# Kernel tuning notes

Measured on AMD Instinct MI355X. Metric: run time of the kernel, lower is better.

Reference implementation:

```python
import jax, jax.numpy as jnp
import numpy as np

N_AUTHOR, N_SUBJECT, N_PAPER = 200000, 50000, 100000
E = 1000000
D = 64
NEG_SLOPE = 0.01


def setup_inputs() -> dict:
    key = jax.random.key(0)
    ks = jax.random.split(key, 16)
    return {
        "feat_author": jax.random.normal(ks[0], (N_AUTHOR, D), jnp.float32),
        "feat_subject": jax.random.normal(ks[1], (N_SUBJECT, D), jnp.float32),
        "feat_paper": jax.random.normal(ks[2], (N_PAPER, D), jnp.float32),
        "edge_src_ap": jax.random.randint(ks[3], (E,), 0, N_AUTHOR, jnp.int32),
        "edge_dst_ap": jax.random.randint(ks[4], (E,), 0, N_PAPER, jnp.int32),
        "edge_src_sp": jax.random.randint(ks[5], (E,), 0, N_SUBJECT, jnp.int32),
        "edge_dst_sp": jax.random.randint(ks[6], (E,), 0, N_PAPER, jnp.int32),
        "attn_l_ap": jax.random.normal(ks[7], (D,), jnp.float32) * 0.1,
        "attn_r_ap": jax.random.normal(ks[8], (D,), jnp.float32) * 0.1,
        "attn_l_sp": jax.random.normal(ks[9], (D,), jnp.float32) * 0.1,
        "attn_r_sp": jax.random.normal(ks[10], (D,), jnp.float32) * 0.1,
        "fc_w": jax.random.normal(ks[11], (D, D), jnp.float32) * 0.1,
        "fc_b": jax.random.normal(ks[12], (D,), jnp.float32) * 0.1,
        "sem_attn": jax.random.normal(ks[13], (D,), jnp.float32) * 0.1,
    }


def heco_gat(feat_src, feat_dst, attn_l, attn_r, src, dst, n_dst):
    # per-node attention logits
    el = feat_src @ attn_l          # [Ns]
    er = feat_dst @ attn_r          # [Nd]
    e = el[src] + er[dst]           # [E]
    e = jnp.where(e > 0, e, NEG_SLOPE * e)  # leaky_relu
    # edge softmax grouped by destination node (numerically stable)
    emax = jax.ops.segment_max(e, dst, num_segments=n_dst)
    ee = jnp.exp(e - emax[dst])
    denom = jax.ops.segment_sum(ee, dst, num_segments=n_dst)
    a = ee / denom[dst]             # [E]
    # weighted scatter-sum aggregation
    out = jax.ops.segment_sum(a[:, None] * feat_src[src], dst, num_segments=n_dst)
    return jax.nn.elu(out)


def semantic_attention(h, fc_w, fc_b, sem_attn):
    # h: [N, M, d]
    w = jnp.tanh(h @ fc_w.T + fc_b).mean(axis=0) @ sem_attn  # [M]
    beta = jax.nn.softmax(w)                                  # [M]
    return jnp.einsum("m,nmd->nd", beta, h)


def reference(feat_author, feat_subject, feat_paper,
              edge_src_ap, edge_dst_ap, edge_src_sp, edge_dst_sp,
              attn_l_ap, attn_r_ap, attn_l_sp, attn_r_sp,
              fc_w, fc_b, sem_attn):
    n_dst = feat_paper.shape[0]
    h_ap = heco_gat(feat_author, feat_paper, attn_l_ap, attn_r_ap,
                    edge_src_ap, edge_dst_ap, n_dst)
    h_sp = heco_gat(feat_subject, feat_paper, attn_l_sp, attn_r_sp,
                    edge_src_sp, edge_dst_sp, n_dst)
    h = jnp.stack([h_ap, h_sp], axis=1)  # [N_dst, 2, D]
    return semantic_attention(h, fc_w, fc_b, sem_attn)
```

## Files before the change

kernel.cpp:

```cpp
#include <hip/hip_runtime.h>
#include <math.h>

#define N_AUTHOR 200000
#define N_SUBJECT 50000
#define N_PAPER 100000
#define NEDGE 1000000
#define D 64
#define NEG_SLOPE 0.01f

#define NSLOT (2 * N_PAPER)
#define CAP 40
#define DROWS (N_AUTHOR + N_SUBJECT + N_PAPER)

__device__ __forceinline__ float bcast(float v, int lane) {
    return __uint_as_float((unsigned)__builtin_amdgcn_readlane(__float_as_int(v), lane));
}
__device__ __forceinline__ int bcast_i(int v, int lane) {
    return __builtin_amdgcn_readlane(v, lane);
}
__device__ __forceinline__ float fast_tanh(float x) {
    x = fminf(15.0f, fmaxf(-15.0f, x));
    float ex = __expf(2.0f * x);
    return (ex - 1.0f) / (ex + 1.0f);
}


__global__ void dots_scatter_kernel(const float* __restrict__ fa,
                                    const float* __restrict__ fs,
                                    const float* __restrict__ fp,
                                    const float* __restrict__ al_ap,
                                    const float* __restrict__ ar_ap,
                                    const float* __restrict__ al_sp,
                                    const float* __restrict__ ar_sp,
                                    float* __restrict__ el_ap,
                                    float* __restrict__ el_sp,
                                    float* __restrict__ er_ap,
                                    float* __restrict__ er_sp,
                                    const int* __restrict__ src_ap,
                                    const int* __restrict__ dst_ap,
                                    const int* __restrict__ src_sp,
                                    const int* __restrict__ dst_sp,
                                    int* __restrict__ count,
                                    int* __restrict__ bucket,
                                    int nb_dots) {
    if ((int)blockIdx.x < nb_dots) {
        int row  = blockIdx.x * 4 + (threadIdx.x >> 6);
        int lane = threadIdx.x & 63;
        if (row < N_AUTHOR) {
            float v = fa[(size_t)row * D + lane] * al_ap[lane];
#pragma unroll
            for (int o = 32; o > 0; o >>= 1) v += __shfl_xor(v, o, 64);
            if (lane == 0) el_ap[row] = v;
        } else if (row < N_AUTHOR + N_SUBJECT) {
            int r = row - N_AUTHOR;
            float v = fs[(size_t)r * D + lane] * al_sp[lane];
#pragma unroll
            for (int o = 32; o > 0; o >>= 1) v += __shfl_xor(v, o, 64);
            if (lane == 0) el_sp[r] = v;
        } else if (row < DROWS) {
            int r = row - (N_AUTHOR + N_SUBJECT);
            float f  = fp[(size_t)r * D + lane];
            float v0 = f * ar_ap[lane];
            float v1 = f * ar_sp[lane];
#pragma unroll
            for (int o = 32; o > 0; o >>= 1) {
                v0 += __shfl_xor(v0, o, 64);
                v1 += __shfl_xor(v1, o, 64);
            }
            if (lane == 0) { er_ap[r] = v0; er_sp[r] = v1; }
        }
    } else {
        const int nthreads = 2 * NEDGE / 4;
        int tid = (blockIdx.x - nb_dots) * blockDim.x + threadIdx.x;
        if (tid >= nthreads) return;
#pragma unroll
        for (int k = 0; k < 4; ++k) {
            int i = tid + k * nthreads;
            int s, dslot;
            if (i < NEDGE) {
                s = src_ap[i];
                dslot = dst_ap[i];
            } else {
                int j = i - NEDGE;
                s = src_sp[j];
                dslot = N_PAPER + dst_sp[j];
            }
            int pos = atomicAdd(&count[dslot], 1);
            if (pos < CAP) bucket[dslot * CAP + pos] = s;
        }
    }
}

__global__ void __launch_bounds__(256, 4)
node_gat_fused_kernel(const int* __restrict__ count,
                      const int* __restrict__ bucket,
                      const float* __restrict__ el_ap,
                      const float* __restrict__ el_sp,
                      const float* __restrict__ er_ap,
                      const float* __restrict__ er_sp,
                      const float* __restrict__ feat_author,
                      const float* __restrict__ feat_subject,
                      float* __restrict__ h_ap,
                      float* __restrict__ h_sp,
                      const float* __restrict__ fc_w,
                      const float* __restrict__ fc_b,
                      const float* __restrict__ sem_attn,
                      float* __restrict__ wsum) {
    __shared__ float red[8];
    int wid  = threadIdx.x >> 6;
    int lane = threadIdx.x & 63;

    float fw[D];
    {
        const float4* fw4 = (const float4*)(fc_w + (size_t)lane * D);
#pragma unroll
        for (int k = 0; k < 16; ++k) {
            float4 v = fw4[k];
            fw[4 * k + 0] = v.x; fw[4 * k + 1] = v.y;
            fw[4 * k + 2] = v.z; fw[4 * k + 3] = v.w;
        }
    }
    float fb = fc_b[lane];
    float sa = sem_attn[lane];
    float taccL0 = 0.0f, taccL1 = 0.0f;

    for (int slot = blockIdx.x * 4 + wid; slot < NSLOT; slot += gridDim.x * 4) {
        int mp = slot >= N_PAPER;
        const float* feat = mp ? feat_subject : feat_author;
        const float* el   = mp ? el_sp : el_ap;
        float er_s = mp ? er_sp[slot - N_PAPER] : er_ap[slot];
        int len = count[slot];
        len = len < CAP ? len : CAP;

        int   sreg = 0;
        float ev   = -1e30f;
        if (lane < len) {
            sreg = bucket[slot * CAP + lane];
            float e = el[sreg] + er_s;
            ev = e > 0.0f ? e : NEG_SLOPE * e;
        }
        float m = ev;
#pragma unroll
        for (int o = 32; o > 0; o >>= 1) m = fmaxf(m, __shfl_xor(m, o, 64));
        float w = (lane < len) ? __expf(ev - m) : 0.0f;
        float sden = w;
#pragma unroll
        for (int o = 32; o > 0; o >>= 1) sden += __shfl_xor(sden, o, 64);

        float a0 = 0.0f, a1 = 0.0f, a2 = 0.0f, a3 = 0.0f;
        int j = 0;
        for (; j + 4 <= len; j += 4) {
            float w0 = bcast(w, j),     w1 = bcast(w, j + 1);
            float w2 = bcast(w, j + 2), w3 = bcast(w, j + 3);
            int   s0 = bcast_i(sreg, j),     s1 = bcast_i(sreg, j + 1);
            int   s2 = bcast_i(sreg, j + 2), s3 = bcast_i(sreg, j + 3);
            a0 = fmaf(w0, feat[(size_t)s0 * D + lane], a0);
            a1 = fmaf(w1, feat[(size_t)s1 * D + lane], a1);
            a2 = fmaf(w2, feat[(size_t)s2 * D + lane], a2);
            a3 = fmaf(w3, feat[(size_t)s3 * D + lane], a3);
        }
        for (; j < len; ++j) {
            float w0 = bcast(w, j);
            int   s0 = bcast_i(sreg, j);
            a0 = fmaf(w0, feat[(size_t)s0 * D + lane], a0);
        }
        float hpre = len ? (((a0 + a1) + (a2 + a3)) / sden) : 0.0f;
        float hv = hpre > 0.0f ? hpre : (__expf(hpre) - 1.0f);

        float* h = mp ? (h_sp + (size_t)(slot - N_PAPER) * D)
                      : (h_ap + (size_t)slot * D);
        h[lane] = hv;

        float m0 = 0.0f, m1 = 0.0f, m2 = 0.0f, m3 = 0.0f;
#pragma unroll
        for (int dd = 0; dd < D; dd += 4) {
            m0 = fmaf(bcast(hv, dd),     fw[dd],     m0);
            m1 = fmaf(bcast(hv, dd + 1), fw[dd + 1], m1);
            m2 = fmaf(bcast(hv, dd + 2), fw[dd + 2], m2);
            m3 = fmaf(bcast(hv, dd + 3), fw[dd + 3], m3);
        }
        float y = fb + ((m0 + m1) + (m2 + m3));
        float t = fast_tanh(y) * sa;
        if (mp) taccL1 += t; else taccL0 += t;
    }

#pragma unroll
    for (int o = 32; o > 0; o >>= 1) {
        taccL0 += __shfl_xor(taccL0, o, 64);
        taccL1 += __shfl_xor(taccL1, o, 64);
    }
    if (lane == 0) { red[wid] = taccL0; red[4 + wid] = taccL1; }
    __syncthreads();
    if (threadIdx.x == 0) atomicAdd(&wsum[0], red[0] + red[1] + red[2] + red[3]);
    if (threadIdx.x == 1) atomicAdd(&wsum[1], red[4] + red[5] + red[6] + red[7]);
}

__global__ void final_combine_kernel(float4* __restrict__ out,
                                     const float4* __restrict__ h_sp,
                                     const float* __restrict__ wsum,
                                     int n_vec4) {
    int i = blockIdx.x * blockDim.x + threadIdx.x;
    if (i >= n_vec4) return;
    float w0 = wsum[0] * (1.0f / N_PAPER);
    float w1 = wsum[1] * (1.0f / N_PAPER);
    float mx = fmaxf(w0, w1);
    float e0 = __expf(w0 - mx), e1 = __expf(w1 - mx);
    float inv = 1.0f / (e0 + e1);
    float b0 = e0 * inv, b1 = e1 * inv;
    float4 a = out[i], b = h_sp[i];
    out[i] = make_float4(b0 * a.x + b1 * b.x, b0 * a.y + b1 * b.y,
                         b0 * a.z + b1 * b.z, b0 * a.w + b1 * b.w);
}


extern "C" void kernel_launch(void* const* d_in, const int* in_sizes, int n_in,
                              void* d_out, int out_size, void* d_ws, size_t ws_size,
                              hipStream_t stream) {
    const float* feat_author = (const float*)d_in[0];
    const float* feat_subject= (const float*)d_in[1];
    const float* feat_paper  = (const float*)d_in[2];
    const int*   src_ap      = (const int*)d_in[3];
    const int*   dst_ap      = (const int*)d_in[4];
    const int*   src_sp      = (const int*)d_in[5];
    const int*   dst_sp      = (const int*)d_in[6];
    const float* attn_l_ap   = (const float*)d_in[7];
    const float* attn_r_ap   = (const float*)d_in[8];
    const float* attn_l_sp   = (const float*)d_in[9];
    const float* attn_r_sp   = (const float*)d_in[10];
    const float* fc_w        = (const float*)d_in[11];
    const float* fc_b        = (const float*)d_in[12];
    const float* sem_attn    = (const float*)d_in[13];

    float* out = (float*)d_out;

    char* ws = (char*)d_ws;
    size_t off = 0;
    auto alloc = [&](size_t bytes) {
        size_t r = off;
        off = (off + bytes + 255) & ~(size_t)255;
        return r;
    };
    int*   count  = (int*)(ws + alloc((size_t)NSLOT * 4));
    float* wsum   = (float*)(ws + alloc(2 * 4));
    size_t zero_bytes = off;
    float* el_ap  = (float*)(ws + alloc((size_t)N_AUTHOR * 4));
    float* er_ap  = (float*)(ws + alloc((size_t)N_PAPER * 4));
    float* el_sp  = (float*)(ws + alloc((size_t)N_SUBJECT * 4));
    float* er_sp  = (float*)(ws + alloc((size_t)N_PAPER * 4));
    int*   bucket = (int*)(ws + alloc((size_t)NSLOT * CAP * 4));
    float* h_sp   = (float*)(ws + alloc((size_t)N_PAPER * D * 4));
    (void)ws_size; (void)in_sizes; (void)n_in;

    hipMemsetAsync(d_ws, 0, zero_bytes, stream);

    const int B = 256;

    int nb_dots    = (DROWS + 3) / 4;
    int nb_scatter = (2 * NEDGE / 4 + B - 1) / B;
    dots_scatter_kernel<<<nb_dots + nb_scatter, B, 0, stream>>>(
        feat_author, feat_subject, feat_paper,
        attn_l_ap, attn_r_ap, attn_l_sp, attn_r_sp,
        el_ap, el_sp, er_ap, er_sp,
        src_ap, dst_ap, src_sp, dst_sp,
        count, bucket, nb_dots);

    node_gat_fused_kernel<<<2048, B, 0, stream>>>(count, bucket,
                                                  el_ap, el_sp, er_ap, er_sp,
                                                  feat_author, feat_subject,
                                                  out, h_sp,
                                                  fc_w, fc_b, sem_attn, wsum);

    int n_vec4 = N_PAPER * D / 4;
    final_combine_kernel<<<(n_vec4 + B - 1) / B, B, 0, stream>>>(
        (float4*)out, (const float4*)h_sp, wsum, n_vec4);
}
```

Measured before the change: 538.4 us.

## Split metapath pipeline to overlap subject-edge scatter with author-paper GAT

Restructures the launch sequence into three kernels. The first scatters author-paper edges and computes the node dot products. The second scatters subject-paper edges while other blocks run GAT aggregation for the author metapath. The third runs GAT for the subject metapath. This lets atomic scatter work overlap with gather/aggregation work instead of serialising all scatter before all GAT. It also switches bucket writes to nontemporal stores. The cost is an extra kernel launch and a duplicated fc_w register load per kernel.

```diff
diff --git a/kernel.cpp b/kernel.cpp
--- a/kernel.cpp
+++ b/kernel.cpp
@@ -11,6 +11,7 @@
 #define NSLOT (2 * N_PAPER)
 #define CAP 40
 #define DROWS (N_AUTHOR + N_SUBJECT + N_PAPER)
+#define NB_SCAT 977
 
 __device__ __forceinline__ float bcast(float v, int lane) {
     return __uint_as_float((unsigned)__builtin_amdgcn_readlane(__float_as_int(v), lane));
@@ -24,92 +25,143 @@
     return (ex - 1.0f) / (ex + 1.0f);
 }
 
-
-__global__ void dots_scatter_kernel(const float* __restrict__ fa,
-                                    const float* __restrict__ fs,
-                                    const float* __restrict__ fp,
-                                    const float* __restrict__ al_ap,
-                                    const float* __restrict__ ar_ap,
-                                    const float* __restrict__ al_sp,
-                                    const float* __restrict__ ar_sp,
-                                    float* __restrict__ el_ap,
-                                    float* __restrict__ el_sp,
-                                    float* __restrict__ er_ap,
-                                    float* __restrict__ er_sp,
-                                    const int* __restrict__ src_ap,
-                                    const int* __restrict__ dst_ap,
-                                    const int* __restrict__ src_sp,
-                                    const int* __restrict__ dst_sp,
-                                    int* __restrict__ count,
-                                    int* __restrict__ bucket,
-                                    int nb_dots) {
-    if ((int)blockIdx.x < nb_dots) {
-        int row  = blockIdx.x * 4 + (threadIdx.x >> 6);
-        int lane = threadIdx.x & 63;
-        if (row < N_AUTHOR) {
-            float v = fa[(size_t)row * D + lane] * al_ap[lane];
-#pragma unroll
-            for (int o = 32; o > 0; o >>= 1) v += __shfl_xor(v, o, 64);
-            if (lane == 0) el_ap[row] = v;
-        } else if (row < N_AUTHOR + N_SUBJECT) {
-            int r = row - N_AUTHOR;
-            float v = fs[(size_t)r * D + lane] * al_sp[lane];
-#pragma unroll
-            for (int o = 32; o > 0; o >>= 1) v += __shfl_xor(v, o, 64);
-            if (lane == 0) el_sp[r] = v;
-        } else if (row < DROWS) {
-            int r = row - (N_AUTHOR + N_SUBJECT);
-            float f  = fp[(size_t)r * D + lane];
-            float v0 = f * ar_ap[lane];
-            float v1 = f * ar_sp[lane];
-#pragma unroll
-            for (int o = 32; o > 0; o >>= 1) {
-                v0 += __shfl_xor(v0, o, 64);
-                v1 += __shfl_xor(v1, o, 64);
-            }
-            if (lane == 0) { er_ap[r] = v0; er_sp[r] = v1; }
+__device__ __forceinline__ void scatter_edges(const int* __restrict__ src,
+                                              const int* __restrict__ dst,
+                                              int* __restrict__ count,
+                                              int* __restrict__ bucket,
+                                              int base, int tid) {
+    const int nthreads = NEDGE / 4;
+    if (tid >= nthreads) return;
+#pragma unroll
+    for (int k = 0; k < 4; ++k) {
+        int i = tid + k * nthreads;
+        int s = src[i];
+        int dslot = base + dst[i];
+        int pos = atomicAdd(&count[dslot], 1);
+        if (pos < CAP)
+            __builtin_nontemporal_store(s, &bucket[(size_t)dslot * CAP + pos]);
+    }
+}
+
+__device__ __forceinline__ float gat_slot(int slot,
+                                          const int* __restrict__ count,
+                                          const int* __restrict__ bucket,
+                                          const float* __restrict__ el,
+                                          const float* __restrict__ er,
+                                          const float* __restrict__ feat,
+                                          float* __restrict__ h,
+                                          const float* fw, float fb, float sa,
+                                          int lane) {
+    float er_s = er[slot];
+    int len = count[slot];
+    len = len < CAP ? len : CAP;
+
+    int   sreg = 0;
+    float ev   = -1e30f;
+    if (lane < len) {
+        sreg = bucket[(size_t)slot * CAP + lane];
+        float e = el[sreg] + er_s;
+        ev = e > 0.0f ? e : NEG_SLOPE * e;
+    }
+    float m = ev;
+#pragma unroll
+    for (int o = 32; o > 0; o >>= 1) m = fmaxf(m, __shfl_xor(m, o, 64));
+    float w = (lane < len) ? __expf(ev - m) : 0.0f;
+    float sden = w;
+#pragma unroll
+    for (int o = 32; o > 0; o >>= 1) sden += __shfl_xor(sden, o, 64);
+
+    float a0 = 0.0f, a1 = 0.0f, a2 = 0.0f, a3 = 0.0f;
+    int j = 0;
+    for (; j + 4 <= len; j += 4) {
+        float w0 = bcast(w, j),     w1 = bcast(w, j + 1);
+        float w2 = bcast(w, j + 2), w3 = bcast(w, j + 3);
+        int   s0 = bcast_i(sreg, j),     s1 = bcast_i(sreg, j + 1);
+        int   s2 = bcast_i(sreg, j + 2), s3 = bcast_i(sreg, j + 3);
+        a0 = fmaf(w0, feat[(size_t)s0 * D + lane], a0);
+        a1 = fmaf(w1, feat[(size_t)s1 * D + lane], a1);
+        a2 = fmaf(w2, feat[(size_t)s2 * D + lane], a2);
+        a3 = fmaf(w3, feat[(size_t)s3 * D + lane], a3);
+    }
+    for (; j < len; ++j) {
+        float w0 = bcast(w, j);
+        int   s0 = bcast_i(sreg, j);
+        a0 = fmaf(w0, feat[(size_t)s0 * D + lane], a0);
+    }
+    float hpre = len ? (((a0 + a1) + (a2 + a3)) / sden) : 0.0f;
+    float hv = hpre > 0.0f ? hpre : (__expf(hpre) - 1.0f);
+
+    h[(size_t)slot * D + lane] = hv;
+
+    float m0 = 0.0f, m1 = 0.0f, m2 = 0.0f, m3 = 0.0f;
+#pragma unroll
+    for (int dd = 0; dd < D; dd += 4) {
+        m0 = fmaf(bcast(hv, dd),     fw[dd],     m0);
+        m1 = fmaf(bcast(hv, dd + 1), fw[dd + 1], m1);
+        m2 = fmaf(bcast(hv, dd + 2), fw[dd + 2], m2);
+        m3 = fmaf(bcast(hv, dd + 3), fw[dd + 3], m3);
+    }
+    float y = fb + ((m0 + m1) + (m2 + m3));
+    return fast_tanh(y) * sa;
+}
+
+__global__ void __launch_bounds__(256, 4)
+k1_scatap_dots(const int* __restrict__ src_ap, const int* __restrict__ dst_ap,
+               int* __restrict__ count, int* __restrict__ bucket,
+               const float* __restrict__ fa, const float* __restrict__ fs,
+               const float* __restrict__ fp,
+               const float* __restrict__ al_ap, const float* __restrict__ ar_ap,
+               const float* __restrict__ al_sp, const float* __restrict__ ar_sp,
+               float* __restrict__ el_ap, float* __restrict__ el_sp,
+               float* __restrict__ er_ap, float* __restrict__ er_sp) {
+    if ((int)blockIdx.x < NB_SCAT) {
+        scatter_edges(src_ap, dst_ap, count, bucket, 0,
+                      blockIdx.x * blockDim.x + threadIdx.x);
+        return;
+    }
+    int row  = (blockIdx.x - NB_SCAT) * 4 + (threadIdx.x >> 6);
+    int lane = threadIdx.x & 63;
+    if (row < N_AUTHOR) {
+        float v = fa[(size_t)row * D + lane] * al_ap[lane];
+#pragma unroll
+        for (int o = 32; o > 0; o >>= 1) v += __shfl_xor(v, o, 64);
+        if (lane == 0) el_ap[row] = v;
+    } else if (row < N_AUTHOR + N_SUBJECT) {
+        int r = row - N_AUTHOR;
+        float v = fs[(size_t)r * D + lane] * al_sp[lane];
+#pragma unroll
+        for (int o = 32; o > 0; o >>= 1) v += __shfl_xor(v, o, 64);
+        if (lane == 0) el_sp[r] = v;
+    } else if (row < DROWS) {
+        int r = row - (N_AUTHOR + N_SUBJECT);
+        float f  = fp[(size_t)r * D + lane];
+        float v0 = f * ar_ap[lane];
+        float v1 = f * ar_sp[lane];
+#pragma unroll
+        for (int o = 32; o > 0; o >>= 1) {
+            v0 += __shfl_xor(v0, o, 64);
+            v1 += __shfl_xor(v1, o, 64);
         }
-    } else {
-        const int nthreads = 2 * NEDGE / 4;
-        int tid = (blockIdx.x - nb_dots) * blockDim.x + threadIdx.x;
-        if (tid >= nthreads) return;
-#pragma unroll
-        for (int k = 0; k < 4; ++k) {
-            int i = tid + k * nthreads;
-            int s, dslot;
-            if (i < NEDGE) {
-                s = src_ap[i];
-                dslot = dst_ap[i];
-            } else {
-                int j = i - NEDGE;
-                s = src_sp[j];
-                dslot = N_PAPER + dst_sp[j];
-            }
-            int pos = atomicAdd(&count[dslot], 1);
-            if (pos < CAP) bucket[dslot * CAP + pos] = s;
-        }
+        if (lane == 0) { er_ap[r] = v0; er_sp[r] = v1; }
     }
 }
 
 __global__ void __launch_bounds__(256, 4)
-node_gat_fused_kernel(const int* __restrict__ count,
-                      const int* __restrict__ bucket,
-                      const float* __restrict__ el_ap,
-                      const float* __restrict__ el_sp,
-                      const float* __restrict__ er_ap,
-                      const float* __restrict__ er_sp,
-                      const float* __restrict__ feat_author,
-                      const float* __restrict__ feat_subject,
-                      float* __restrict__ h_ap,
-                      float* __restrict__ h_sp,
-                      const float* __restrict__ fc_w,
-                      const float* __restrict__ fc_b,
-                      const float* __restrict__ sem_attn,
-                      float* __restrict__ wsum) {
-    __shared__ float red[8];
+k2_scatsp_gatap(const int* __restrict__ src_sp, const int* __restrict__ dst_sp,
+                int* __restrict__ count, int* __restrict__ bucket,
+                const float* __restrict__ el_ap, const float* __restrict__ er_ap,
+                const float* __restrict__ feat_author,
+                float* __restrict__ h_ap,
+                const float* __restrict__ fc_w, const float* __restrict__ fc_b,
+                const float* __restrict__ sem_attn, float* __restrict__ wsum) {
+    if ((int)blockIdx.x < NB_SCAT) {
+        scatter_edges(src_sp, dst_sp, count, bucket, N_PAPER,
+                      blockIdx.x * blockDim.x + threadIdx.x);
+        return;
+    }
+    __shared__ float red[4];
     int wid  = threadIdx.x >> 6;
     int lane = threadIdx.x & 63;
-
     float fw[D];
     {
         const float4* fw4 = (const float4*)(fc_w + (size_t)lane * D);
@@ -122,77 +174,54 @@
     }
     float fb = fc_b[lane];
     float sa = sem_attn[lane];
-    float taccL0 = 0.0f, taccL1 = 0.0f;
-
-    for (int slot = blockIdx.x * 4 + wid; slot < NSLOT; slot += gridDim.x * 4) {
-        int mp = slot >= N_PAPER;
-        const float* feat = mp ? feat_subject : feat_author;
-        const float* el   = mp ? el_sp : el_ap;
-        float er_s = mp ? er_sp[slot - N_PAPER] : er_ap[slot];
-        int len = count[slot];
-        len = len < CAP ? len : CAP;
-
-        int   sreg = 0;
-        float ev   = -1e30f;
-        if (lane < len) {
-            sreg = bucket[slot * CAP + lane];
-            float e = el[sreg] + er_s;
-            ev = e > 0.0f ? e : NEG_SLOPE * e;
+    float tacc = 0.0f;
+    int b2 = blockIdx.x - NB_SCAT;
+    int nb = gridDim.x - NB_SCAT;
+    for (int slot = b2 * 4 + wid; slot < N_PAPER; slot += nb * 4)
+        tacc += gat_slot(slot, count, bucket, el_ap, er_ap,
+                         feat_author, h_ap, fw, fb, sa, lane);
+#pragma unroll
+    for (int o = 32; o > 0; o >>= 1) tacc += __shfl_xor(tacc, o, 64);
+    if (lane == 0) red[wid] = tacc;
+    __syncthreads();
+    if (threadIdx.x == 0)
+        atomicAdd(&wsum[0], red[0] + red[1] + red[2] + red[3]);
+}
+
+__global__ void __launch_bounds__(256, 4)
+k3_gatsp(const int* __restrict__ count, const int* __restrict__ bucket,
+         const float* __restrict__ el_sp, const float* __restrict__ er_sp,
+         const float* __restrict__ feat_subject,
+         float* __restrict__ h_sp,
+         const float* __restrict__ fc_w, const float* __restrict__ fc_b,
+         const float* __restrict__ sem_attn, float* __restrict__ wsum) {
+    __shared__ float red[4];
+    int wid  = threadIdx.x >> 6;
+    int lane = threadIdx.x & 63;
+    float fw[D];
+    {
+        const float4* fw4 = (const float4*)(fc_w + (size_t)lane * D);
+#pragma unroll
+        for (int k = 0; k < 16; ++k) {
+            float4 v = fw4[k];
+            fw[4 * k + 0] = v.x; fw[4 * k + 1] = v.y;
+            fw[4 * k + 2] = v.z; fw[4 * k + 3] = v.w;
         }
-        float m = ev;
-#pragma unroll
-        for (int o = 32; o > 0; o >>= 1) m = fmaxf(m, __shfl_xor(m, o, 64));
-        float w = (lane < len) ? __expf(ev - m) : 0.0f;
-        float sden = w;
-#pragma unroll
-        for (int o = 32; o > 0; o >>= 1) sden += __shfl_xor(sden, o, 64);
-
-        float a0 = 0.0f, a1 = 0.0f, a2 = 0.0f, a3 = 0.0f;
-        int j = 0;
-        for (; j + 4 <= len; j += 4) {
-            float w0 = bcast(w, j),     w1 = bcast(w, j + 1);
-            float w2 = bcast(w, j + 2), w3 = bcast(w, j + 3);
-            int   s0 = bcast_i(sreg, j),     s1 = bcast_i(sreg, j + 1);
-            int   s2 = bcast_i(sreg, j + 2), s3 = bcast_i(sreg, j + 3);
-            a0 = fmaf(w0, feat[(size_t)s0 * D + lane], a0);
-            a1 = fmaf(w1, feat[(size_t)s1 * D + lane], a1);
-            a2 = fmaf(w2, feat[(size_t)s2 * D + lane], a2);
-            a3 = fmaf(w3, feat[(size_t)s3 * D + lane], a3);
-        }
-        for (; j < len; ++j) {
-            float w0 = bcast(w, j);
-            int   s0 = bcast_i(sreg, j);
-            a0 = fmaf(w0, feat[(size_t)s0 * D + lane], a0);
-        }
-        float hpre = len ? (((a0 + a1) + (a2 + a3)) / sden) : 0.0f;
-        float hv = hpre > 0.0f ? hpre : (__expf(hpre) - 1.0f);
-
-        float* h = mp ? (h_sp + (size_t)(slot - N_PAPER) * D)
-                      : (h_ap + (size_t)slot * D);
-        h[lane] = hv;
-
-        float m0 = 0.0f, m1 = 0.0f, m2 = 0.0f, m3 = 0.0f;
-#pragma unroll
-        for (int dd = 0; dd < D; dd += 4) {
-            m0 = fmaf(bcast(hv, dd),     fw[dd],     m0);
-            m1 = fmaf(bcast(hv, dd + 1), fw[dd + 1], m1);
-            m2 = fmaf(bcast(hv, dd + 2), fw[dd + 2], m2);
-            m3 = fmaf(bcast(hv, dd + 3), fw[dd + 3], m3);
-        }
-        float y = fb + ((m0 + m1) + (m2 + m3));
-        float t = fast_tanh(y) * sa;
-        if (mp) taccL1 += t; else taccL0 += t;
-    }
-
-#pragma unroll
-    for (int o = 32; o > 0; o >>= 1) {
-        taccL0 += __shfl_xor(taccL0, o, 64);
-        taccL1 += __shfl_xor(taccL1, o, 64);
-    }
-    if (lane == 0) { red[wid] = taccL0; red[4 + wid] = taccL1; }
+    }
+    float fb = fc_b[lane];
+    float sa = sem_attn[lane];
+    float tacc = 0.0f;
+    const int* count_sp  = count + N_PAPER;
+    const int* bucket_sp = bucket + (size_t)N_PAPER * CAP;
+    for (int s = blockIdx.x * 4 + wid; s < N_PAPER; s += gridDim.x * 4)
+        tacc += gat_slot(s, count_sp, bucket_sp, el_sp, er_sp,
+                         feat_subject, h_sp, fw, fb, sa, lane);
+#pragma unroll
+    for (int o = 32; o > 0; o >>= 1) tacc += __shfl_xor(tacc, o, 64);
+    if (lane == 0) red[wid] = tacc;
     __syncthreads();
-    if (threadIdx.x == 0) atomicAdd(&wsum[0], red[0] + red[1] + red[2] + red[3]);
-    if (threadIdx.x == 1) atomicAdd(&wsum[1], red[4] + red[5] + red[6] + red[7]);
+    if (threadIdx.x == 0)
+        atomicAdd(&wsum[1], red[0] + red[1] + red[2] + red[3]);
 }
 
 __global__ void final_combine_kernel(float4* __restrict__ out,
@@ -255,20 +284,21 @@
 
     const int B = 256;
 
-    int nb_dots    = (DROWS + 3) / 4;
-    int nb_scatter = (2 * NEDGE / 4 + B - 1) / B;
-    dots_scatter_kernel<<<nb_dots + nb_scatter, B, 0, stream>>>(
+    int nb_dots = (DROWS + 3) / 4;
+    k1_scatap_dots<<<NB_SCAT + nb_dots, B, 0, stream>>>(
+        src_ap, dst_ap, count, bucket,
         feat_author, feat_subject, feat_paper,
         attn_l_ap, attn_r_ap, attn_l_sp, attn_r_sp,
-        el_ap, el_sp, er_ap, er_sp,
-        src_ap, dst_ap, src_sp, dst_sp,
-        count, bucket, nb_dots);
-
-    node_gat_fused_kernel<<<2048, B, 0, stream>>>(count, bucket,
-                                                  el_ap, el_sp, er_ap, er_sp,
-                                                  feat_author, feat_subject,
-                                                  out, h_sp,
-                                                  fc_w, fc_b, sem_attn, wsum);
+        el_ap, el_sp, er_ap, er_sp);
+
+    k2_scatsp_gatap<<<NB_SCAT + 2048, B, 0, stream>>>(
+        src_sp, dst_sp, count, bucket,
+        el_ap, er_ap, feat_author, out,
+        fc_w, fc_b, sem_attn, wsum);
+
+    k3_gatsp<<<2048, B, 0, stream>>>(
+        count, bucket, el_sp, er_sp, feat_subject, h_sp,
+        fc_w, fc_b, sem_attn, wsum);
 
     int n_vec4 = N_PAPER * D / 4;
     final_combine_kernel<<<(n_vec4 + B - 1) / B, B, 0, stream>>>(
```

After: 556.6 us. 1.03x slower.
